# Performance work log

Hardware: AMD Instinct MI355X
Metric: run time of the kernel (lower is better)

Reference implementation:

```python
import jax, jax.numpy as jnp
import numpy as np

HEADS = 8
DIM_HEAD = 64
EPS = 1e-5


def _inst_norm_lastdim(t):
    # torch InstanceNorm1d receives [(b h), n, d]; with affine=False it normalizes
    # over the spatial (last) dim d per (b,h,n), biased variance, eps=1e-5.
    mu = jnp.mean(t, axis=-1, keepdims=True)
    var = jnp.mean(jnp.square(t - mu), axis=-1, keepdims=True)
    return (t - mu) * jax.lax.rsqrt(var + EPS)


def setup_inputs() -> dict:
    key = jax.random.key(0)
    k1, k2, k3, k4 = jax.random.split(key, 4)
    b, n, dim = 4, 8192, 256
    inner = HEADS * DIM_HEAD  # 512
    x = jax.random.normal(k1, (b, n, dim), dtype=jnp.float32)
    Wqkv = jax.random.normal(k2, (3 * inner, dim), dtype=jnp.float32) * (1.0 / np.sqrt(dim))
    Wout = jax.random.normal(k3, (dim, inner), dtype=jnp.float32) * (1.0 / np.sqrt(inner))
    bout = jax.random.normal(k4, (dim,), dtype=jnp.float32) * 0.01
    return {"x": x, "Wqkv": Wqkv, "Wout": Wout, "bout": bout}


def reference(x, Wqkv, Wout, bout):
    b, n, dim = x.shape
    qkv = jnp.einsum('bnc,fc->bnf', x, Wqkv)  # [b, n, 3*inner]
    q, k, v = jnp.split(qkv, 3, axis=-1)
    def to_heads(t):
        return t.reshape(b, n, HEADS, DIM_HEAD).transpose(0, 2, 1, 3)  # [b,h,n,d]
    q, k, v = to_heads(q), to_heads(k), to_heads(v)
    # galerkin: instance-norm k and v
    k = _inst_norm_lastdim(k)
    v = _inst_norm_lastdim(v)
    # associative linear attention: (k^T v) then q @ dots, scaled by 1/n
    dots = jnp.einsum('bhnd,bhne->bhde', k, v)        # [b,h,d,d]
    out = jnp.einsum('bhnd,bhde->bhne', q, dots) / n  # [b,h,n,d]
    out = out.transpose(0, 2, 1, 3).reshape(b, n, HEADS * DIM_HEAD)
    return jnp.einsum('bnf,cf->bnc', out, Wout) + bout
```

## Files before the change

kernel.cpp:

```cpp
#include <hip/hip_runtime.h>
#include <hip/hip_bf16.h>

#define SEQ    8192
#define NROWS  32768
#define EPS    1e-5f

typedef __attribute__((ext_vector_type(4))) float f32x4;
typedef __attribute__((ext_vector_type(8))) short bf16x8;
typedef __attribute__((ext_vector_type(8))) unsigned short u16x8;

__device__ __forceinline__ unsigned short f2bu(float f) {
  __hip_bfloat16 h = __float2bfloat16(f);
  return __builtin_bit_cast(unsigned short, h);
}
__device__ __forceinline__ float b2f(unsigned short u) {
  return __bfloat162float(__builtin_bit_cast(__hip_bfloat16, u));
}

__global__ __launch_bounds__(256) void convert_kernel(const float* __restrict__ in,
                                                      unsigned short* __restrict__ out, int n4) {
  int i = blockIdx.x * 256 + threadIdx.x;
  if (i >= n4) return;
  float4 v = reinterpret_cast<const float4*>(in)[i];
  ushort4 o;
  o.x = f2bu(v.x); o.y = f2bu(v.y); o.z = f2bu(v.z); o.w = f2bu(v.w);
  reinterpret_cast<ushort4*>(out)[i] = o;
}

__global__ __launch_bounds__(256) void wprep_kernel(const float* __restrict__ W,
                                                    unsigned short* __restrict__ wb,
                                                    unsigned short* __restrict__ wqT) {
  int i = blockIdx.x * 256 + threadIdx.x;
  if (i >= 98304) return;
  float4 v = reinterpret_cast<const float4*>(W)[i];
  ushort4 o;
  o.x = f2bu(v.x); o.y = f2bu(v.y); o.z = f2bu(v.z); o.w = f2bu(v.w);
  reinterpret_cast<ushort4*>(wb)[i] = o;
  const int e = i * 4;
  const int f = e >> 8;
  if (f < 512) {
    const int c = e & 255;
    wqT[(size_t)(c + 0) * 512 + f] = o.x;
    wqT[(size_t)(c + 1) * 512 + f] = o.y;
    wqT[(size_t)(c + 2) * 512 + f] = o.z;
    wqT[(size_t)(c + 3) * 512 + f] = o.w;
  }
}

template<int K, int LDA, int LDC, bool PERB, bool BIAS, bool OUTF32>
__global__ __launch_bounds__(256) void gemm_kernel(const unsigned short* __restrict__ A,
                                                   const unsigned short* __restrict__ Bw,
                                                   const float* __restrict__ bias,
                                                   void* __restrict__ Cout) {
  __shared__ char smem[32768];
  unsigned short* As = (unsigned short*)smem;
  unsigned short* Bs = (unsigned short*)(smem + 16384);
  const int row0 = blockIdx.y * 128;
  const int col0 = blockIdx.x * 128;
  const unsigned short* Bp = Bw;
  if constexpr (PERB) Bp += (size_t)(row0 >> 13) * (size_t)(LDC * K);
  const int tid  = threadIdx.x;
  const int lane = tid & 63;
  const int wave = tid >> 6;
  const int wr = (wave >> 1) << 6;
  const int wc = (wave & 1) << 6;
  const int srow = tid >> 3;
  const int scol = (tid & 7) << 3;

  f32x4 acc[4][4] = {};

  for (int k0 = 0; k0 < K; k0 += 64) {
#pragma unroll
    for (int it = 0; it < 4; ++it) {
      const unsigned short* ga = A + (size_t)(row0 + it * 32 + srow) * LDA + (k0 + scol);
      __builtin_amdgcn_global_load_lds(
          (const __attribute__((address_space(1))) void*)ga,
          (__attribute__((address_space(3))) void*)((char*)As + (it * 4096 + wave * 1024)),
          16, 0, 0);
      const unsigned short* gb = Bp + (size_t)(col0 + it * 32 + srow) * K + (k0 + scol);
      __builtin_amdgcn_global_load_lds(
          (const __attribute__((address_space(1))) void*)gb,
          (__attribute__((address_space(3))) void*)((char*)Bs + (it * 4096 + wave * 1024)),
          16, 0, 0);
    }
    __syncthreads();
#pragma unroll
    for (int ks = 0; ks < 2; ++ks) {
      bf16x8 af[4], bfr[4];
#pragma unroll
      for (int mt = 0; mt < 4; ++mt)
        af[mt] = *reinterpret_cast<const bf16x8*>(
            &As[(wr + mt * 16 + (lane & 15)) * 64 + ks * 32 + (lane >> 4) * 8]);
#pragma unroll
      for (int nt = 0; nt < 4; ++nt)
        bfr[nt] = *reinterpret_cast<const bf16x8*>(
            &Bs[(wc + nt * 16 + (lane & 15)) * 64 + ks * 32 + (lane >> 4) * 8]);
#pragma unroll
      for (int mt = 0; mt < 4; ++mt)
#pragma unroll
        for (int nt = 0; nt < 4; ++nt)
          acc[mt][nt] = __builtin_amdgcn_mfma_f32_16x16x32_bf16(af[mt], bfr[nt], acc[mt][nt], 0, 0, 0);
    }
    __syncthreads();
  }

  if constexpr (OUTF32) {
#pragma unroll
    for (int mt = 0; mt < 4; ++mt) {
#pragma unroll
      for (int nt = 0; nt < 4; ++nt) {
        const int col = col0 + wc + nt * 16 + (lane & 15);
        float bv = 0.0f;
        if constexpr (BIAS) bv = bias[col];
#pragma unroll
        for (int i = 0; i < 4; ++i) {
          const int row = row0 + wr + mt * 16 + ((lane >> 4) << 2) + i;
          reinterpret_cast<float*>(Cout)[(size_t)row * LDC + col] = acc[mt][nt][i] + bv;
        }
      }
    }
  } else {
    unsigned short* Ct = (unsigned short*)smem;
#pragma unroll
    for (int mt = 0; mt < 4; ++mt) {
#pragma unroll
      for (int nt = 0; nt < 4; ++nt) {
        const int lc = wc + nt * 16 + (lane & 15);
        float bv = 0.0f;
        if constexpr (BIAS) bv = bias[col0 + lc];
#pragma unroll
        for (int i = 0; i < 4; ++i) {
          const int lr = wr + mt * 16 + ((lane >> 4) << 2) + i;
          Ct[lr * 128 + lc] = f2bu(acc[mt][nt][i] + bv);
        }
      }
    }
    __syncthreads();
    const int r = tid >> 1, cs = (tid & 1) << 6;
    unsigned short* gout = (unsigned short*)Cout + (size_t)(row0 + r) * LDC + col0 + cs;
    const unsigned short* lsrc = Ct + r * 128 + cs;
#pragma unroll
    for (int i = 0; i < 8; ++i)
      *reinterpret_cast<u16x8*>(gout + i * 8) = *reinterpret_cast<const u16x8*>(lsrc + i * 8);
  }
}

__global__ __launch_bounds__(256) void dots_kernel(const unsigned short* __restrict__ kvb,
                                                   float* __restrict__ partial) {
  const int bh = blockIdx.x;
  const int chunk = blockIdx.y;
  const int b = bh >> 3, h = bh & 7;
  const int t = threadIdx.x;
  __shared__ float lbuf[2][4360];

  const int r  = t >> 3;
  const int j  = t & 7;
  const int kv = j >> 2;
  const int jj = j & 3;
  const int dq = t & 15;
  const int eq = t >> 4;

  const size_t rowbase = (size_t)(b * SEQ + chunk * 512 + r) * 1024 + kv * 512 + h * 64 + jj * 16;
  const int lds_off = kv * 2180 + r * 68 + jj * 16;

  float acc[4][4] = {};
  u16x8 raw0, raw1;
  raw0 = *reinterpret_cast<const u16x8*>(kvb + rowbase);
  raw1 = *reinterpret_cast<const u16x8*>(kvb + rowbase + 8);

  int p = 0;
  {
    float x[16];
#pragma unroll
    for (int i = 0; i < 8; ++i) { x[i] = b2f(raw0[i]); x[8 + i] = b2f(raw1[i]); }
    float s = 0.f, s2 = 0.f;
#pragma unroll
    for (int i = 0; i < 16; ++i) { s += x[i]; s2 += x[i] * x[i]; }
    s += __shfl_xor(s, 1, 64);  s2 += __shfl_xor(s2, 1, 64);
    s += __shfl_xor(s, 2, 64);  s2 += __shfl_xor(s2, 2, 64);
    const float mean = s * (1.0f / 64.0f);
    float var = s2 * (1.0f / 64.0f) - mean * mean;
    var = var < 0.f ? 0.f : var;
    const float rs = rsqrtf(var + EPS);
    float* dst = &lbuf[0][lds_off];
#pragma unroll
    for (int i = 0; i < 4; ++i) {
      f32x4 o = { (x[4*i+0]-mean)*rs, (x[4*i+1]-mean)*rs, (x[4*i+2]-mean)*rs, (x[4*i+3]-mean)*rs };
      *reinterpret_cast<f32x4*>(dst + 4 * i) = o;
    }
  }

  for (int sIt = 0; sIt < 16; ++sIt) {
    const bool more = (sIt + 1) < 16;
    if (more) {
      const unsigned short* src = kvb + rowbase + (size_t)(sIt + 1) * 32 * 1024;
      raw0 = *reinterpret_cast<const u16x8*>(src);
      raw1 = *reinterpret_cast<const u16x8*>(src + 8);
    }
    __syncthreads();
    {
      const float* lk = &lbuf[p][0];
      const float* lv = &lbuf[p][2180];
#pragma unroll 4
      for (int rr = 0; rr < 32; ++rr) {
        f32x4 kf = *reinterpret_cast<const f32x4*>(lk + rr * 68 + dq * 4);
        f32x4 vf = *reinterpret_cast<const f32x4*>(lv + rr * 68 + eq * 4);
#pragma unroll
        for (int i = 0; i < 4; ++i)
#pragma unroll
          for (int jx = 0; jx < 4; ++jx)
            acc[i][jx] = fmaf(kf[i], vf[jx], acc[i][jx]);
      }
    }
    if (more) {
      float x[16];
#pragma unroll
      for (int i = 0; i < 8; ++i) { x[i] = b2f(raw0[i]); x[8 + i] = b2f(raw1[i]); }
      float s = 0.f, s2 = 0.f;
#pragma unroll
      for (int i = 0; i < 16; ++i) { s += x[i]; s2 += x[i] * x[i]; }
      s += __shfl_xor(s, 1, 64);  s2 += __shfl_xor(s2, 1, 64);
      s += __shfl_xor(s, 2, 64);  s2 += __shfl_xor(s2, 2, 64);
      const float mean = s * (1.0f / 64.0f);
      float var = s2 * (1.0f / 64.0f) - mean * mean;
      var = var < 0.f ? 0.f : var;
      const float rs = rsqrtf(var + EPS);
      float* dst = &lbuf[p ^ 1][lds_off];
#pragma unroll
      for (int i = 0; i < 4; ++i) {
        f32x4 o = { (x[4*i+0]-mean)*rs, (x[4*i+1]-mean)*rs, (x[4*i+2]-mean)*rs, (x[4*i+3]-mean)*rs };
        *reinterpret_cast<f32x4*>(dst + 4 * i) = o;
      }
    }
    p ^= 1;
  }

  float* pp = partial + ((size_t)(chunk * 32 + bh) << 12) + (size_t)(dq * 4) * 64 + eq * 4;
#pragma unroll
  for (int i = 0; i < 4; ++i) {
    f32x4 o = { acc[i][0], acc[i][1], acc[i][2], acc[i][3] };
    *reinterpret_cast<f32x4*>(pp + i * 64) = o;
  }
}

__global__ __launch_bounds__(256) void reduce_kernel(const float* __restrict__ partial,
                                                     float* __restrict__ dots) {
  const int i = blockIdx.x * 256 + threadIdx.x;
  f32x4 s = {};
#pragma unroll
  for (int c = 0; c < 16; ++c)
    s += reinterpret_cast<const f32x4*>(partial)[(size_t)c * 32768 + i];
  reinterpret_cast<f32x4*>(dots)[i] = s;
}

__global__ __launch_bounds__(512) void m2_kernel(const float* __restrict__ dots,
                                                 const float* __restrict__ Wout,
                                                 unsigned short* __restrict__ M2) {
  const int b = blockIdx.x;
  const int c = blockIdx.y;
  const int t = threadIdx.x;
  __shared__ float wrow[512];
  wrow[t] = Wout[(size_t)c * 512 + t];
  __syncthreads();
  const int h = t >> 6, d = t & 63;
  const float* dp = dots + (size_t)(b * 8 + h) * 4096 + (size_t)d * 64;
  float s = 0.0f;
#pragma unroll 8
  for (int e = 0; e < 64; ++e) s += dp[e] * wrow[(h << 6) + e];
  M2[((size_t)b * 256 + c) * 512 + t] = f2bu(s * (1.0f / 8192.0f));
}

extern "C" void kernel_launch(void* const* d_in, const int* in_sizes, int n_in,
                              void* d_out, int out_size, void* d_ws, size_t ws_size,
                              hipStream_t stream) {
  const float* x    = (const float*)d_in[0];
  const float* Wqkv = (const float*)d_in[1];
  const float* Wout = (const float*)d_in[2];
  const float* bout = (const float*)d_in[3];
  char* ws = (char*)d_ws;
  unsigned short* xb    = (unsigned short*)(ws);
  unsigned short* wqkvb = (unsigned short*)(ws + 16777216);
  unsigned short* wqT   = (unsigned short*)(ws + 17563648);
  unsigned short* kvb   = (unsigned short*)(ws + 17825792);
  float*          part  = (float*)         (ws + 84934656);
  float*          dots  = (float*)         (ws + 93323264);
  unsigned short* m2    = (unsigned short*)(ws + 93847552);
  unsigned short* w3    = (unsigned short*)(ws + 94896128);

  convert_kernel<<<dim3(8192), 256, 0, stream>>>(x, xb, 2097152);
  wprep_kernel<<<dim3(384), 256, 0, stream>>>(Wqkv, wqkvb, wqT);
  gemm_kernel<256, 256, 1024, false, false, false><<<dim3(8, 256), 256, 0, stream>>>(
      xb, wqkvb + (size_t)512 * 256, nullptr, kvb);
  dots_kernel<<<dim3(32, 16), 256, 0, stream>>>(kvb, part);
  reduce_kernel<<<dim3(128), 256, 0, stream>>>(part, dots);
  m2_kernel<<<dim3(4, 256), 512, 0, stream>>>(dots, Wout, m2);
  gemm_kernel<512, 512, 256, false, false, false><<<dim3(2, 8), 256, 0, stream>>>(m2, wqT, nullptr, w3);
  gemm_kernel<256, 256, 256, true, true, true><<<dim3(2, 256), 256, 0, stream>>>(xb, w3, bout, d_out);
}
```

Before: 218.8 us.

## Load full-K tiles into swizzled LDS with XCD-aware block mapping, merge prep kernels

```diff
diff --git a/kernel.cpp b/kernel.cpp
--- a/kernel.cpp
+++ b/kernel.cpp
@@ -2,7 +2,6 @@
 #include <hip/hip_bf16.h>
 
 #define SEQ    8192
-#define NROWS  32768
 #define EPS    1e-5f
 
 typedef __attribute__((ext_vector_type(4))) float f32x4;
@@ -17,48 +16,153 @@
   return __bfloat162float(__builtin_bit_cast(__hip_bfloat16, u));
 }
 
-__global__ __launch_bounds__(256) void convert_kernel(const float* __restrict__ in,
-                                                      unsigned short* __restrict__ out, int n4) {
-  int i = blockIdx.x * 256 + threadIdx.x;
-  if (i >= n4) return;
-  float4 v = reinterpret_cast<const float4*>(in)[i];
-  ushort4 o;
-  o.x = f2bu(v.x); o.y = f2bu(v.y); o.z = f2bu(v.z); o.w = f2bu(v.w);
-  reinterpret_cast<ushort4*>(out)[i] = o;
-}
-
-__global__ __launch_bounds__(256) void wprep_kernel(const float* __restrict__ W,
-                                                    unsigned short* __restrict__ wb,
-                                                    unsigned short* __restrict__ wqT) {
-  int i = blockIdx.x * 256 + threadIdx.x;
-  if (i >= 98304) return;
-  float4 v = reinterpret_cast<const float4*>(W)[i];
-  ushort4 o;
-  o.x = f2bu(v.x); o.y = f2bu(v.y); o.z = f2bu(v.z); o.w = f2bu(v.w);
-  reinterpret_cast<ushort4*>(wb)[i] = o;
-  const int e = i * 4;
-  const int f = e >> 8;
-  if (f < 512) {
-    const int c = e & 255;
-    wqT[(size_t)(c + 0) * 512 + f] = o.x;
-    wqT[(size_t)(c + 1) * 512 + f] = o.y;
-    wqT[(size_t)(c + 2) * 512 + f] = o.z;
-    wqT[(size_t)(c + 3) * 512 + f] = o.w;
-  }
-}
-
-template<int K, int LDA, int LDC, bool PERB, bool BIAS, bool OUTF32>
+__global__ __launch_bounds__(256) void prep_kernel(const float* __restrict__ x,
+                                                   const float* __restrict__ W,
+                                                   unsigned short* __restrict__ xb,
+                                                   unsigned short* __restrict__ wb,
+                                                   unsigned short* __restrict__ wqT) {
+  const int bid = blockIdx.x;
+  const int t = threadIdx.x;
+  if (bid < 8192) {
+    const int i = bid * 256 + t;
+    float4 v = reinterpret_cast<const float4*>(x)[i];
+    ushort4 o;
+    o.x = f2bu(v.x); o.y = f2bu(v.y); o.z = f2bu(v.z); o.w = f2bu(v.w);
+    reinterpret_cast<ushort4*>(xb)[i] = o;
+  } else {
+    const int i = (bid - 8192) * 256 + t;
+    float4 v = reinterpret_cast<const float4*>(W)[i];
+    ushort4 o;
+    o.x = f2bu(v.x); o.y = f2bu(v.y); o.z = f2bu(v.z); o.w = f2bu(v.w);
+    reinterpret_cast<ushort4*>(wb)[i] = o;
+    const int e = i * 4;
+    const int f = e >> 8;
+    if (f < 512) {
+      const int c = e & 255;
+      wqT[(size_t)(c + 0) * 512 + f] = o.x;
+      wqT[(size_t)(c + 1) * 512 + f] = o.y;
+      wqT[(size_t)(c + 2) * 512 + f] = o.z;
+      wqT[(size_t)(c + 3) * 512 + f] = o.w;
+    }
+  }
+}
+
+template<int NCB, int NRP, bool PERB, bool BIAS, bool OUTF32, int LDC>
+__global__ __launch_bounds__(512) void gemm_fullk(const unsigned short* __restrict__ A,
+                                                  const unsigned short* __restrict__ Bw,
+                                                  const float* __restrict__ bias,
+                                                  void* __restrict__ Cout) {
+  extern __shared__ char smem[];
+  unsigned short* As = (unsigned short*)smem;
+  unsigned short* Bs = (unsigned short*)(smem + 65536);
+  const int lin = blockIdx.x;
+  const int xcd = lin & 7;
+  const int loc = lin >> 3;
+  const int cb  = loc % NCB;
+  const int rp  = xcd * (NRP / 8) + loc / NCB;
+  const int row0 = rp * 128;
+  const int col0 = cb * 128;
+  const unsigned short* Bp = Bw;
+  if constexpr (PERB) Bp += (size_t)(row0 >> 13) * (size_t)(LDC * 256);
+  const int tid  = threadIdx.x;
+  const int lane = tid & 63;
+  const int wave = tid >> 6;
+
+  {
+    const int srow = tid >> 5;
+    const int cb16 = (tid & 31) << 4;
+#pragma unroll
+    for (int it = 0; it < 8; ++it) {
+      const int row = it * 16 + srow;
+      const int src_cb = cb16 ^ ((row & 7) << 4);
+      const unsigned short* ga = A + (size_t)(row0 + row) * 256 + (src_cb >> 1);
+      __builtin_amdgcn_global_load_lds(
+          (const __attribute__((address_space(1))) void*)ga,
+          (__attribute__((address_space(3))) void*)(smem + it * 8192 + tid * 16), 16, 0, 0);
+      const unsigned short* gb = Bp + (size_t)(col0 + row) * 256 + (src_cb >> 1);
+      __builtin_amdgcn_global_load_lds(
+          (const __attribute__((address_space(1))) void*)gb,
+          (__attribute__((address_space(3))) void*)(smem + 65536 + it * 8192 + tid * 16), 16, 0, 0);
+    }
+  }
+  __syncthreads();
+
+  const int wr = (wave >> 2) << 6;
+  const int wc = (wave & 3) << 5;
+  f32x4 acc[4][2] = {};
+#pragma unroll
+  for (int ks = 0; ks < 8; ++ks) {
+    bf16x8 af[4], bfr[2];
+#pragma unroll
+    for (int mt = 0; mt < 4; ++mt) {
+      const int r = wr + mt * 16 + (lane & 15);
+      const int cbyt = (ks * 64 + ((lane >> 4) << 4)) ^ ((r & 7) << 4);
+      af[mt] = *reinterpret_cast<const bf16x8*>(As + r * 256 + (cbyt >> 1));
+    }
+#pragma unroll
+    for (int nt = 0; nt < 2; ++nt) {
+      const int c = wc + nt * 16 + (lane & 15);
+      const int cbyt = (ks * 64 + ((lane >> 4) << 4)) ^ ((c & 7) << 4);
+      bfr[nt] = *reinterpret_cast<const bf16x8*>(Bs + c * 256 + (cbyt >> 1));
+    }
+#pragma unroll
+    for (int mt = 0; mt < 4; ++mt)
+#pragma unroll
+      for (int nt = 0; nt < 2; ++nt)
+        acc[mt][nt] = __builtin_amdgcn_mfma_f32_16x16x32_bf16(af[mt], bfr[nt], acc[mt][nt], 0, 0, 0);
+  }
+
+  if constexpr (OUTF32) {
+#pragma unroll
+    for (int mt = 0; mt < 4; ++mt) {
+#pragma unroll
+      for (int nt = 0; nt < 2; ++nt) {
+        const int colg = col0 + wc + nt * 16 + (lane & 15);
+        float bv = 0.0f;
+        if constexpr (BIAS) bv = bias[colg];
+#pragma unroll
+        for (int i = 0; i < 4; ++i) {
+          const int rowg = row0 + wr + mt * 16 + ((lane >> 4) << 2) + i;
+          reinterpret_cast<float*>(Cout)[(size_t)rowg * LDC + colg] = acc[mt][nt][i] + bv;
+        }
+      }
+    }
+  } else {
+    __syncthreads();
+    unsigned short* Ct = (unsigned short*)smem;
+#pragma unroll
+    for (int mt = 0; mt < 4; ++mt) {
+#pragma unroll
+      for (int nt = 0; nt < 2; ++nt) {
+        const int lc = wc + nt * 16 + (lane & 15);
+        float bv = 0.0f;
+        if constexpr (BIAS) bv = bias[col0 + lc];
+#pragma unroll
+        for (int i = 0; i < 4; ++i) {
+          const int lr = wr + mt * 16 + ((lane >> 4) << 2) + i;
+          Ct[lr * 128 + lc] = f2bu(acc[mt][nt][i] + bv);
+        }
+      }
+    }
+    __syncthreads();
+    const int r = tid >> 2, cs = (tid & 3) << 5;
+    unsigned short* gout = (unsigned short*)Cout + (size_t)(row0 + r) * LDC + col0 + cs;
+    const unsigned short* lsrc = Ct + r * 128 + cs;
+#pragma unroll
+    for (int i = 0; i < 4; ++i)
+      *reinterpret_cast<u16x8*>(gout + i * 8) = *reinterpret_cast<const u16x8*>(lsrc + i * 8);
+  }
+}
+
+template<int K, int LDA, int LDC>
 __global__ __launch_bounds__(256) void gemm_kernel(const unsigned short* __restrict__ A,
                                                    const unsigned short* __restrict__ Bw,
-                                                   const float* __restrict__ bias,
                                                    void* __restrict__ Cout) {
-  __shared__ char smem[32768];
-  unsigned short* As = (unsigned short*)smem;
-  unsigned short* Bs = (unsigned short*)(smem + 16384);
+  __shared__ char smem2[32768];
+  unsigned short* As = (unsigned short*)smem2;
+  unsigned short* Bs = (unsigned short*)(smem2 + 16384);
   const int row0 = blockIdx.y * 128;
   const int col0 = blockIdx.x * 128;
-  const unsigned short* Bp = Bw;
-  if constexpr (PERB) Bp += (size_t)(row0 >> 13) * (size_t)(LDC * K);
   const int tid  = threadIdx.x;
   const int lane = tid & 63;
   const int wave = tid >> 6;
@@ -66,22 +170,18 @@
   const int wc = (wave & 1) << 6;
   const int srow = tid >> 3;
   const int scol = (tid & 7) << 3;
-
   f32x4 acc[4][4] = {};
-
   for (int k0 = 0; k0 < K; k0 += 64) {
 #pragma unroll
     for (int it = 0; it < 4; ++it) {
       const unsigned short* ga = A + (size_t)(row0 + it * 32 + srow) * LDA + (k0 + scol);
       __builtin_amdgcn_global_load_lds(
           (const __attribute__((address_space(1))) void*)ga,
-          (__attribute__((address_space(3))) void*)((char*)As + (it * 4096 + wave * 1024)),
-          16, 0, 0);
-      const unsigned short* gb = Bp + (size_t)(col0 + it * 32 + srow) * K + (k0 + scol);
+          (__attribute__((address_space(3))) void*)((char*)As + (it * 4096 + wave * 1024)), 16, 0, 0);
+      const unsigned short* gb = Bw + (size_t)(col0 + it * 32 + srow) * K + (k0 + scol);
       __builtin_amdgcn_global_load_lds(
           (const __attribute__((address_space(1))) void*)gb,
-          (__attribute__((address_space(3))) void*)((char*)Bs + (it * 4096 + wave * 1024)),
-          16, 0, 0);
+          (__attribute__((address_space(3))) void*)((char*)Bs + (it * 4096 + wave * 1024)), 16, 0, 0);
     }
     __syncthreads();
 #pragma unroll
@@ -103,46 +203,17 @@
     }
     __syncthreads();
   }
-
-  if constexpr (OUTF32) {
-#pragma unroll
-    for (int mt = 0; mt < 4; ++mt) {
-#pragma unroll
-      for (int nt = 0; nt < 4; ++nt) {
-        const int col = col0 + wc + nt * 16 + (lane & 15);
-        float bv = 0.0f;
-        if constexpr (BIAS) bv = bias[col];
-#pragma unroll
-        for (int i = 0; i < 4; ++i) {
-          const int row = row0 + wr + mt * 16 + ((lane >> 4) << 2) + i;
-          reinterpret_cast<float*>(Cout)[(size_t)row * LDC + col] = acc[mt][nt][i] + bv;
-        }
-      }
-    }
-  } else {
-    unsigned short* Ct = (unsigned short*)smem;
-#pragma unroll
-    for (int mt = 0; mt < 4; ++mt) {
-#pragma unroll
-      for (int nt = 0; nt < 4; ++nt) {
-        const int lc = wc + nt * 16 + (lane & 15);
-        float bv = 0.0f;
-        if constexpr (BIAS) bv = bias[col0 + lc];
-#pragma unroll
-        for (int i = 0; i < 4; ++i) {
-          const int lr = wr + mt * 16 + ((lane >> 4) << 2) + i;
-          Ct[lr * 128 + lc] = f2bu(acc[mt][nt][i] + bv);
-        }
-      }
-    }
-    __syncthreads();
-    const int r = tid >> 1, cs = (tid & 1) << 6;
-    unsigned short* gout = (unsigned short*)Cout + (size_t)(row0 + r) * LDC + col0 + cs;
-    const unsigned short* lsrc = Ct + r * 128 + cs;
-#pragma unroll
-    for (int i = 0; i < 8; ++i)
-      *reinterpret_cast<u16x8*>(gout + i * 8) = *reinterpret_cast<const u16x8*>(lsrc + i * 8);
-  }
+#pragma unroll
+  for (int mt = 0; mt < 4; ++mt)
+#pragma unroll
+    for (int nt = 0; nt < 4; ++nt) {
+      const int col = col0 + wc + nt * 16 + (lane & 15);
+#pragma unroll
+      for (int i = 0; i < 4; ++i) {
+        const int row = row0 + wr + mt * 16 + ((lane >> 4) << 2) + i;
+        reinterpret_cast<unsigned short*>(Cout)[(size_t)row * LDC + col] = f2bu(acc[mt][nt][i]);
+      }
+    }
 }
 
 __global__ __launch_bounds__(256) void dots_kernel(const unsigned short* __restrict__ kvb,
@@ -287,13 +358,18 @@
   unsigned short* m2    = (unsigned short*)(ws + 93847552);
   unsigned short* w3    = (unsigned short*)(ws + 94896128);
 
-  convert_kernel<<<dim3(8192), 256, 0, stream>>>(x, xb, 2097152);
-  wprep_kernel<<<dim3(384), 256, 0, stream>>>(Wqkv, wqkvb, wqT);
-  gemm_kernel<256, 256, 1024, false, false, false><<<dim3(8, 256), 256, 0, stream>>>(
+  hipFuncSetAttribute((const void*)gemm_fullk<8, 256, false, false, false, 1024>,
+                      hipFuncAttributeMaxDynamicSharedMemorySize, 131072);
+  hipFuncSetAttribute((const void*)gemm_fullk<2, 256, true, true, true, 256>,
+                      hipFuncAttributeMaxDynamicSharedMemorySize, 131072);
+
+  prep_kernel<<<dim3(8576), 256, 0, stream>>>(x, Wqkv, xb, wqkvb, wqT);
+  gemm_fullk<8, 256, false, false, false, 1024><<<dim3(2048), 512, 131072, stream>>>(
       xb, wqkvb + (size_t)512 * 256, nullptr, kvb);
   dots_kernel<<<dim3(32, 16), 256, 0, stream>>>(kvb, part);
   reduce_kernel<<<dim3(128), 256, 0, stream>>>(part, dots);
   m2_kernel<<<dim3(4, 256), 512, 0, stream>>>(dots, Wout, m2);
-  gemm_kernel<512, 512, 256, false, false, false><<<dim3(2, 8), 256, 0, stream>>>(m2, wqT, nullptr, w3);
-  gemm_kernel<256, 256, 256, true, true, true><<<dim3(2, 256), 256, 0, stream>>>(xb, w3, bout, d_out);
-}
+  gemm_kernel<512, 512, 256><<<dim3(2, 8), 256, 0, stream>>>(m2, wqT, w3);
+  gemm_fullk<2, 256, true, true, true, 256><<<dim3(512), 512, 131072, stream>>>(
+      xb, w3, bout, d_out);
+}
```

Result: no change. 220.6 us (+0.8%).
